# Optimization experiments

Hardware: AMD Instinct MI355X
Metric: run time of the kernel (lower is better)

Reference implementation:

```python
import jax, jax.numpy as jnp
import numpy as np


def setup_inputs() -> dict:
    key = jax.random.key(0)
    k1, k2, k3 = jax.random.split(key, 3)
    b_n, f_num, N = 2, 4, 50
    n = b_n * f_num
    C_in, C = 256, 64
    h, w = 200, 336
    return {
        "x": jax.random.normal(k1, (n, C, h * w), jnp.float32),
        "idx_feat": jax.random.normal(k2, (n, C_in, N, 1), jnp.float32),
        "weight": jax.random.normal(k3, (C, C_in), jnp.float32) * 0.01,
        "bias": jnp.zeros((C,), jnp.float32),
        "thing_gt_idx": jnp.ones((b_n, N, f_num), jnp.int32),
        "h": h,
        "w": w,
    }


def _con_loss(mw, b_n, N, f_num, C):
    # mw: (b_n*f_num, C, N, 1) kernel embeddings after embed_extractor
    K = N * f_num
    # reshape/permute mirrors torch: (b_n, N, f_num, C) flattened row-major ->
    # rows ordered (instance, frame), matching the boolean-mask gather order
    # under a dense (all-ones) thing_gt_idx mask.
    m = mw.reshape(b_n, f_num, C, N).transpose(0, 3, 1, 2).reshape(b_n, K, C)
    # F.normalize(dim=1)
    m = m / jnp.maximum(jnp.linalg.norm(m, axis=-1, keepdims=True), 1e-12)
    sim = jnp.einsum('bkc,blc->bkl', m, m)  # (b_n, K, K)
    labels = np.repeat(np.arange(N), f_num)  # instance id per row (static)
    f_own = np.tile(np.arange(f_num), N)     # frame id per row (static)
    # static negative gather indices: all columns of other instances, padded by
    # repeating the last negative (torch's while-loop torch.cat) to length K-1
    neg_cols = []
    for i in range(N):
        cols = np.nonzero(labels != i)[0]
        neg_cols.append(np.concatenate([cols, np.full(f_num - 1, cols[-1])]))
    neg_idx = np.stack(neg_cols)[labels]     # (K, K-1)
    # random positive among the f_num-1 same-instance / other-frame entries
    r = jax.random.randint(jax.random.key(42), (b_n, K), 0, f_num - 1)
    pos_off = jnp.where(r >= f_own[None, :], r + 1, r)
    pos_col = labels[None, :] * f_num + pos_off  # (b_n, K)
    positives = sim[jnp.arange(b_n)[:, None], jnp.arange(K)[None, :], pos_col]
    negatives = sim[:, np.arange(K)[:, None], neg_idx]  # (b_n, K, K-1)
    logits = jnp.concatenate([positives[..., None], negatives], axis=-1) / 0.07
    # CrossEntropyLoss with target 0, mean over K rows, summed over batches
    lse = jax.scipy.special.logsumexp(logits, axis=-1)
    return jnp.sum(jnp.mean(lse - logits[..., 0], axis=-1))


def reference(x, idx_feat, weight, bias, thing_gt_idx, h, w):
    b_n, N, f_num = thing_gt_idx.shape
    n = b_n * f_num
    C = weight.shape[0]
    # embed_extractor: 1x1 conv == channel matmul
    mw = jnp.einsum('bcnk,dc->bdnk', idx_feat, weight) + bias[None, :, None, None]
    loss = _con_loss(mw, b_n, N, f_num, C)
    # shuffle_times == 1 branch: kernels @ encoded features
    kernels = mw.reshape(n, C, N).transpose(0, 2, 1)  # (n, N, C)
    inst_pred = jnp.matmul(kernels, x).reshape(n, N, h, w)
    return inst_pred, loss
```

## Files before the change

kernel.cpp:

```cpp
#include <hip/hip_runtime.h>
#include <stdint.h>
#include <float.h>
#include <math.h>

#define HW_TOT 67200
#define NBF 8
#define CO 64
#define CI 256
#define NN 50
#define KK 200
#define BN 2

__device__ __forceinline__ uint32_t rotl32(uint32_t v, int n) {
  return (v << n) | (v >> (32 - n));
}

__device__ void tf2x32(uint32_t k0, uint32_t k1, uint32_t x0, uint32_t x1,
                       uint32_t& o0, uint32_t& o1) {
  const uint32_t ks2 = k0 ^ k1 ^ 0x1BD11BDAu;
  x0 += k0; x1 += k1;
  x0 += x1; x1 = rotl32(x1, 13); x1 ^= x0;
  x0 += x1; x1 = rotl32(x1, 15); x1 ^= x0;
  x0 += x1; x1 = rotl32(x1, 26); x1 ^= x0;
  x0 += x1; x1 = rotl32(x1, 6);  x1 ^= x0;
  x0 += k1; x1 += ks2 + 1u;
  x0 += x1; x1 = rotl32(x1, 17); x1 ^= x0;
  x0 += x1; x1 = rotl32(x1, 29); x1 ^= x0;
  x0 += x1; x1 = rotl32(x1, 16); x1 ^= x0;
  x0 += x1; x1 = rotl32(x1, 24); x1 ^= x0;
  x0 += ks2; x1 += k0 + 2u;
  x0 += x1; x1 = rotl32(x1, 13); x1 ^= x0;
  x0 += x1; x1 = rotl32(x1, 15); x1 ^= x0;
  x0 += x1; x1 = rotl32(x1, 26); x1 ^= x0;
  x0 += x1; x1 = rotl32(x1, 6);  x1 ^= x0;
  x0 += k0; x1 += k1 + 3u;
  x0 += x1; x1 = rotl32(x1, 17); x1 ^= x0;
  x0 += x1; x1 = rotl32(x1, 29); x1 ^= x0;
  x0 += x1; x1 = rotl32(x1, 16); x1 ^= x0;
  x0 += x1; x1 = rotl32(x1, 24); x1 ^= x0;
  x0 += k1; x1 += ks2 + 4u;
  x0 += x1; x1 = rotl32(x1, 13); x1 ^= x0;
  x0 += x1; x1 = rotl32(x1, 15); x1 ^= x0;
  x0 += x1; x1 = rotl32(x1, 26); x1 ^= x0;
  x0 += x1; x1 = rotl32(x1, 6);  x1 ^= x0;
  o0 = x0 + ks2;
  o1 = x1 + k0 + 5u;
}

__device__ int jax_r(int b, int k) {
  uint32_t k1a, k1b, k2a, k2b, h0, h1, l0, l1;
  tf2x32(0u, 42u, 0u, 0u, k1a, k1b);
  tf2x32(0u, 42u, 0u, 1u, k2a, k2b);
  const uint32_t idx = (uint32_t)(b * KK + k);
  tf2x32(k1a, k1b, 0u, idx, h0, h1);
  tf2x32(k2a, k2b, 0u, idx, l0, l1);
  const uint32_t hb = h0 ^ h1, lb = l0 ^ l1;
  return (int)(((hb % 3u) + (lb % 3u)) % 3u);
}

__global__ __launch_bounds__(256) void k_mw(const float* __restrict__ idx_feat,
                                            const float* __restrict__ weight,
                                            const float* __restrict__ bias,
                                            float* __restrict__ mw) {
  const int tid = blockIdx.x * 256 + threadIdx.x;
  if (tid >= NBF * CO * NN) return;
  const int n = tid % NN;
  const int rest = tid / NN;
  const int d = rest % CO;
  const int b = rest / CO;
  float acc = bias[d];
  const float* feat = idx_feat + (size_t)(b * CI) * NN + n;
  const float* wrow = weight + d * CI;
  #pragma unroll 8
  for (int ci = 0; ci < CI; ++ci)
    acc = fmaf(feat[ci * NN], wrow[ci], acc);
  mw[tid] = acc;
}

__device__ __forceinline__ float waveMax(float v) {
  #pragma unroll
  for (int o = 32; o > 0; o >>= 1) v = fmaxf(v, __shfl_down(v, o));
  return v;
}
__device__ __forceinline__ float waveSum(float v) {
  #pragma unroll
  for (int o = 32; o > 0; o >>= 1) v += __shfl_down(v, o);
  return v;
}

__global__ __launch_bounds__(256) void k_loss(const float* __restrict__ mw,
                                              float* __restrict__ partial) {
  __shared__ __align__(16) float m_lds[KK][68];
  __shared__ float red[8];
  __shared__ float pos_sh;
  __shared__ int rvals[32];

  const int b = blockIdx.x >> 3;
  const int chunk = blockIdx.x & 7;
  const int t = threadIdx.x;
  const int wid = t >> 6, lane = t & 63;
  const int kbase = chunk * 25;

  if (t < 25) rvals[t] = jax_r(b, kbase + t);

  float row[CO];
  if (t < KK) {
    const int f = t & 3, ni = t >> 2;
    const float* src = mw + (size_t)((b * 4 + f) * CO) * NN + ni;
    float ssq = 0.f;
    #pragma unroll
    for (int c = 0; c < CO; ++c) { const float v = src[c * NN]; row[c] = v; ssq += v * v; }
    const float inv = 1.0f / fmaxf(sqrtf(ssq), 1e-12f);
    #pragma unroll
    for (int c = 0; c < CO; ++c) { row[c] *= inv; m_lds[t][c] = row[c]; }
  }
  __syncthreads();

  float part = 0.f;
  for (int kk = 0; kk < 25; ++kk) {
    const int k = kbase + kk;
    const int g = k >> 2, fo = k & 3;
    const int r = rvals[kk];
    const int pos_off = (r >= fo) ? r + 1 : r;
    const int pos_col = (g << 2) + pos_off;
    const int last_neg = (g == NN - 1) ? (KK - 5) : (KK - 1);

    float dot = 0.f;
    if (t < KK) {
      const float4* mk = reinterpret_cast<const float4*>(&m_lds[k][0]);
      #pragma unroll
      for (int c4 = 0; c4 < 16; ++c4) {
        const float4 a = mk[c4];
        dot = fmaf(a.x, row[4 * c4 + 0], dot);
        dot = fmaf(a.y, row[4 * c4 + 1], dot);
        dot = fmaf(a.z, row[4 * c4 + 2], dot);
        dot = fmaf(a.w, row[4 * c4 + 3], dot);
      }
    }
    const float logit = dot * (1.0f / 0.07f);

    float wgt = 0.f;
    if (t < KK) {
      if (t == pos_col) wgt = 1.f;
      else if ((t >> 2) != g) wgt = (t == last_neg) ? 4.f : 1.f;
    }
    const bool valid = wgt > 0.f;

    const float wmax = waveMax(valid ? logit : -FLT_MAX);
    if (lane == 0) red[wid] = wmax;
    if (t == pos_col) pos_sh = logit;
    __syncthreads();
    const float mx = fmaxf(fmaxf(red[0], red[1]), fmaxf(red[2], red[3]));
    const float pos = pos_sh;
    const float ws = waveSum(valid ? wgt * expf(logit - mx) : 0.f);
    if (lane == 0) red[4 + wid] = ws;
    __syncthreads();
    if (t == 0) {
      const float s = red[4] + red[5] + red[6] + red[7];
      part += (mx + logf(s)) - pos;
    }
    __syncthreads();
  }
  if (t == 0) partial[blockIdx.x] = part;
}

#define REP50(M) \
  M(0) M(1) M(2) M(3) M(4) M(5) M(6) M(7) M(8) M(9) \
  M(10) M(11) M(12) M(13) M(14) M(15) M(16) M(17) M(18) M(19) \
  M(20) M(21) M(22) M(23) M(24) M(25) M(26) M(27) M(28) M(29) \
  M(30) M(31) M(32) M(33) M(34) M(35) M(36) M(37) M(38) M(39) \
  M(40) M(41) M(42) M(43) M(44) M(45) M(46) M(47) M(48) M(49)

#define ACC_DECL(i) float acc##i = 0.f;
#define ACC_FMA(i)  acc##i = fmaf(kr[i], xv, acc##i);
#define ACC_ST(i)   ob[(size_t)(i) * HW_TOT] = acc##i;

__global__ __launch_bounds__(256, 4) void k_pred(const float* __restrict__ x,
                                                 const float* __restrict__ mw,
                                                 const float* __restrict__ partial,
                                                 float* __restrict__ out) {
  const int b = blockIdx.y;
  const int p = blockIdx.x * 256 + threadIdx.x;

  if (blockIdx.x == 0 && b == 0 && threadIdx.x == 0) {
    float s = 0.f;
    #pragma unroll
    for (int i = 0; i < 16; ++i) s += partial[i];
    out[(size_t)NBF * NN * HW_TOT] = s * (1.0f / KK);
  }
  if (p >= HW_TOT) return;

  REP50(ACC_DECL)

  const float* xb = x + (size_t)b * CO * HW_TOT + p;
  const float* mwb = mw + b * CO * NN;
  #pragma clang loop unroll_count(2)
  for (int c = 0; c < CO; ++c) {
    const float xv = xb[(size_t)c * HW_TOT];
    const float* kr = mwb + c * NN;
    REP50(ACC_FMA)
  }

  float* ob = out + (size_t)b * NN * HW_TOT + p;
  REP50(ACC_ST)
}

extern "C" void kernel_launch(void* const* d_in, const int* in_sizes, int n_in,
                              void* d_out, int out_size, void* d_ws, size_t ws_size,
                              hipStream_t stream) {
  const float* x        = (const float*)d_in[0];
  const float* idx_feat = (const float*)d_in[1];
  const float* weight   = (const float*)d_in[2];
  const float* bias     = (const float*)d_in[3];
  float* out = (float*)d_out;

  float* mw = (float*)d_ws;
  float* partial = mw + NBF * CO * NN;

  hipLaunchKernelGGL(k_mw, dim3((NBF * CO * NN + 255) / 256), dim3(256), 0, stream,
                     idx_feat, weight, bias, mw);
  hipLaunchKernelGGL(k_loss, dim3(16), dim3(256), 0, stream, mw, partial);
  hipLaunchKernelGGL(k_pred, dim3((HW_TOT + 255) / 256, NBF), dim3(256), 0, stream,
                     x, mw, partial, out);
}
```

Measured before the change: 98.90 us.

## Split prediction kernel across two halves of instances with nontemporal stores

The per-pixel prediction kernel now computes 25 of the 50 instance outputs per thread, with a third grid dimension selecting which half. This cuts accumulator registers so occupancy can rise (launch bounds raised to 6 blocks), while each x element is read twice. The channel loop is unrolled by four with separate loads, and output stores use nontemporal hints to avoid polluting caches with the large write stream.

```diff
diff --git a/kernel.cpp b/kernel.cpp
--- a/kernel.cpp
+++ b/kernel.cpp
@@ -164,25 +164,27 @@
   if (t == 0) partial[blockIdx.x] = part;
 }
 
-#define REP50(M) \
+#define REP25(M) \
   M(0) M(1) M(2) M(3) M(4) M(5) M(6) M(7) M(8) M(9) \
   M(10) M(11) M(12) M(13) M(14) M(15) M(16) M(17) M(18) M(19) \
-  M(20) M(21) M(22) M(23) M(24) M(25) M(26) M(27) M(28) M(29) \
-  M(30) M(31) M(32) M(33) M(34) M(35) M(36) M(37) M(38) M(39) \
-  M(40) M(41) M(42) M(43) M(44) M(45) M(46) M(47) M(48) M(49)
+  M(20) M(21) M(22) M(23) M(24)
 
 #define ACC_DECL(i) float acc##i = 0.f;
-#define ACC_FMA(i)  acc##i = fmaf(kr[i], xv, acc##i);
-#define ACC_ST(i)   ob[(size_t)(i) * HW_TOT] = acc##i;
-
-__global__ __launch_bounds__(256, 4) void k_pred(const float* __restrict__ x,
+#define ACC_FMA0(i) acc##i = fmaf(kr0[i], xv0, acc##i);
+#define ACC_FMA1(i) acc##i = fmaf(kr1[i], xv1, acc##i);
+#define ACC_FMA2(i) acc##i = fmaf(kr2[i], xv2, acc##i);
+#define ACC_FMA3(i) acc##i = fmaf(kr3[i], xv3, acc##i);
+#define ACC_ST(i)   __builtin_nontemporal_store(acc##i, ob + (size_t)(i) * HW_TOT);
+
+__global__ __launch_bounds__(256, 6) void k_pred(const float* __restrict__ x,
                                                  const float* __restrict__ mw,
                                                  const float* __restrict__ partial,
                                                  float* __restrict__ out) {
   const int b = blockIdx.y;
+  const int half = blockIdx.z;
   const int p = blockIdx.x * 256 + threadIdx.x;
 
-  if (blockIdx.x == 0 && b == 0 && threadIdx.x == 0) {
+  if (blockIdx.x == 0 && b == 0 && half == 0 && threadIdx.x == 0) {
     float s = 0.f;
     #pragma unroll
     for (int i = 0; i < 16; ++i) s += partial[i];
@@ -190,19 +192,29 @@
   }
   if (p >= HW_TOT) return;
 
-  REP50(ACC_DECL)
+  REP25(ACC_DECL)
 
   const float* xb = x + (size_t)b * CO * HW_TOT + p;
-  const float* mwb = mw + b * CO * NN;
+  const float* mwb = mw + b * CO * NN + half * 25;
+
   #pragma clang loop unroll_count(2)
-  for (int c = 0; c < CO; ++c) {
-    const float xv = xb[(size_t)c * HW_TOT];
-    const float* kr = mwb + c * NN;
-    REP50(ACC_FMA)
-  }
-
-  float* ob = out + (size_t)b * NN * HW_TOT + p;
-  REP50(ACC_ST)
+  for (int c = 0; c < CO; c += 4) {
+    const float xv0 = xb[(size_t)(c + 0) * HW_TOT];
+    const float xv1 = xb[(size_t)(c + 1) * HW_TOT];
+    const float xv2 = xb[(size_t)(c + 2) * HW_TOT];
+    const float xv3 = xb[(size_t)(c + 3) * HW_TOT];
+    const float* kr0 = mwb + (c + 0) * NN;
+    const float* kr1 = mwb + (c + 1) * NN;
+    const float* kr2 = mwb + (c + 2) * NN;
+    const float* kr3 = mwb + (c + 3) * NN;
+    REP25(ACC_FMA0)
+    REP25(ACC_FMA1)
+    REP25(ACC_FMA2)
+    REP25(ACC_FMA3)
+  }
+
+  float* ob = out + (size_t)b * NN * HW_TOT + (size_t)half * 25 * HW_TOT + p;
+  REP25(ACC_ST)
 }
 
 extern "C" void kernel_launch(void* const* d_in, const int* in_sizes, int n_in,
@@ -220,6 +232,6 @@
   hipLaunchKernelGGL(k_mw, dim3((NBF * CO * NN + 255) / 256), dim3(256), 0, stream,
                      idx_feat, weight, bias, mw);
   hipLaunchKernelGGL(k_loss, dim3(16), dim3(256), 0, stream, mw, partial);
-  hipLaunchKernelGGL(k_pred, dim3((HW_TOT + 255) / 256, NBF), dim3(256), 0, stream,
+  hipLaunchKernelGGL(k_pred, dim3((HW_TOT + 255) / 256, NBF, 2), dim3(256), 0, stream,
                      x, mw, partial, out);
 }
```

New measurement: 125.3 us. +26.7%, slower.
